# Kernel optimization log

Measured on AMD Instinct MI355X. Metric: run time of the kernel, lower is better.

## Reference

```python
import jax, jax.numpy as jnp
import numpy as np

EMB = 1024
HEADS = 16
HEAD_DIM = EMB // HEADS
ROPE_BASE = 10000.0


def rotate_half(x):
    # Interleaved rotate: pairs (x0,x1,x2,x3,...) -> (-x1,x0,-x3,x2,...)
    x1 = x[..., ::2]
    x2 = x[..., 1::2]
    return jnp.stack((-x2, x1), axis=-1).reshape(x.shape)


def rope_cos_sin(seq_len, head_dim):
    inv_freq = 1.0 / (ROPE_BASE ** (jnp.arange(0, head_dim, 2, dtype=jnp.float32) / head_dim))
    pos = jnp.arange(seq_len, dtype=jnp.float32)
    freqs = jnp.outer(pos, inv_freq)            # [S, hd/2]
    emb = jnp.concatenate([freqs, freqs], -1)   # [S, hd]  (NOTE: concat, matching source)
    return jnp.cos(emb)[None, None], jnp.sin(emb)[None, None]  # [1,1,S,hd]


def setup_inputs() -> dict:
    key = jax.random.key(0)
    ks = jax.random.split(key, 5)
    B, S = 2, 2048
    x = jax.random.normal(ks[0], (B, S, EMB), dtype=jnp.float32)
    scale = EMB ** -0.5
    Wq = jax.random.normal(ks[1], (EMB, EMB), dtype=jnp.float32) * scale
    Wk = jax.random.normal(ks[2], (EMB, EMB), dtype=jnp.float32) * scale
    Wv = jax.random.normal(ks[3], (EMB, EMB), dtype=jnp.float32) * scale
    Wo = jax.random.normal(ks[4], (EMB, EMB), dtype=jnp.float32) * scale
    return {"x": x, "Wq": Wq, "Wk": Wk, "Wv": Wv, "Wo": Wo}


def reference(x, Wq, Wk, Wv, Wo):
    B, S, E = x.shape
    def shape_heads(t):
        return t.reshape(B, S, HEADS, HEAD_DIM).transpose(0, 2, 1, 3)  # [B,H,S,hd]
    q = shape_heads(x @ Wq.T)
    k = shape_heads(x @ Wk.T)
    v = shape_heads(x @ Wv.T)
    cos, sin = rope_cos_sin(S, HEAD_DIM)
    q = q * cos + rotate_half(q) * sin
    k = k * cos + rotate_half(k) * sin
    scale = HEAD_DIM ** -0.5
    scores = jnp.einsum('bhqd,bhkd->bhqk', q, k) * scale  # [B,H,S,S]
    causal = jnp.triu(jnp.ones((S, S), dtype=bool), k=1)
    scores = jnp.where(causal, -jnp.inf, scores)
    attn = jax.nn.softmax(scores, axis=-1)
    out = jnp.einsum('bhqk,bhkd->bhqd', attn, v)           # [B,H,S,hd]
    out = out.transpose(0, 2, 1, 3).reshape(B, S, E)
    return out @ Wo.T
```

## Files before the change

kernel.cpp:

```cpp
#include <hip/hip_runtime.h>
#include <cstdint>
#include <cstddef>

typedef __bf16 bf16;
typedef __attribute__((ext_vector_type(8))) __bf16 bf16x8;
typedef __attribute__((ext_vector_type(4))) __bf16 bf16x4;
typedef __attribute__((ext_vector_type(4))) float f32x4;

constexpr int kS = 2048;
constexpr int kH = 16;
constexpr int kD = 64;

__device__ __forceinline__ void gload16(const bf16* g, bf16* l) {
  __builtin_amdgcn_global_load_lds((const __attribute__((address_space(1))) void*)g,
                                   (__attribute__((address_space(3))) void*)l, 16, 0, 0);
}

__global__ __launch_bounds__(256) void cast_all_kernel(
    const float* __restrict__ x, const float* __restrict__ wq, const float* __restrict__ wk,
    const float* __restrict__ wv, const float* __restrict__ wo,
    bf16* __restrict__ xb, bf16* __restrict__ wqb, bf16* __restrict__ wkb,
    bf16* __restrict__ wvb, bf16* __restrict__ wob) {
  int idx = blockIdx.x * 256 + threadIdx.x;
  const float* src; bf16* dst; int i;
  if (idx < (1 << 20)) { src = x; dst = xb; i = idx << 2; }
  else {
    int r = idx - (1 << 20);
    int t = r >> 18;
    i = (r & ((1 << 18) - 1)) << 2;
    src = (t == 0) ? wq : (t == 1) ? wk : (t == 2) ? wv : wo;
    dst = (t == 0) ? wqb : (t == 1) ? wkb : (t == 2) ? wvb : wob;
  }
  float4 v = *(const float4*)(src + i);
  bf16x4 o;
  o[0] = (bf16)v.x; o[1] = (bf16)v.y; o[2] = (bf16)v.z; o[3] = (bf16)v.w;
  *(bf16x4*)(dst + i) = o;
}


#define GSTAGE(BUF, KT)                                    \
  gload16(aP0 + (KT), &As[BUF][(w * 64 + l) * 8]);         \
  gload16(aP1 + (KT), &As[BUF][((4 + w) * 64 + l) * 8]);   \
  gload16(bP0 + (KT), &Bs[BUF][(w * 64 + l) * 8]);         \
  gload16(bP1 + (KT), &Bs[BUF][((4 + w) * 64 + l) * 8]);

__global__ __launch_bounds__(256) void gemm_qkv(const bf16* __restrict__ A,
                                                const bf16* __restrict__ wq,
                                                const bf16* __restrict__ wk,
                                                const bf16* __restrict__ wv,
                                                bf16* __restrict__ qo,
                                                bf16* __restrict__ ko,
                                                bf16* __restrict__ vto) {
  __shared__ bf16 As[2][128 * 32];
  __shared__ bf16 Bs[2][128 * 32];
  const int tid = threadIdx.x;
  const int w = tid >> 6, l = tid & 63;
  const int wr = w >> 1, wc = w & 1;
  const int lr = l & 15, lg = l >> 4;

  const int fid = (blockIdx.x & 7) * 96 + (blockIdx.x >> 3);
  const int mblk = fid & 31;
  const int ntile = fid >> 5;
  const int which = ntile >> 3;
  const int m0 = mblk * 128;
  const int n0 = (ntile & 7) * 128;
  const bf16* Bw = (which == 0) ? wq : (which == 1) ? wk : wv;

  const int srow = l >> 2;
  const int skcol = ((l & 3) ^ ((l >> 3) & 3)) << 3;
  const int K = 1024;

  const bf16* aP0 = A + (size_t)(m0 + w * 16 + srow) * K + skcol;
  const bf16* aP1 = A + (size_t)(m0 + 64 + w * 16 + srow) * K + skcol;
  const bf16* bP0 = Bw + (size_t)(n0 + w * 16 + srow) * K + skcol;
  const bf16* bP1 = Bw + (size_t)(n0 + 64 + w * 16 + srow) * K + skcol;

  f32x4 acc[4][4] = {};
  const int ca = (lg ^ ((lr >> 1) & 3)) * 8;

  GSTAGE(0, 0)
  __syncthreads();
  int cur = 0;
  for (int kt = 0; kt < K; kt += 32) {
    if (kt + 32 < K) { GSTAGE(cur ^ 1, kt + 32) }
    bf16x8 af[4], bfg[4];
#pragma unroll
    for (int mi = 0; mi < 4; mi++)
      af[mi] = *(const bf16x8*)&As[cur][(wr * 64 + mi * 16 + lr) * 32 + ca];
#pragma unroll
    for (int ni = 0; ni < 4; ni++)
      bfg[ni] = *(const bf16x8*)&Bs[cur][(wc * 64 + ni * 16 + lr) * 32 + ca];
    __builtin_amdgcn_s_setprio(1);
#pragma unroll
    for (int mi = 0; mi < 4; mi++)
#pragma unroll
      for (int ni = 0; ni < 4; ni++)
        acc[mi][ni] = __builtin_amdgcn_mfma_f32_16x16x32_bf16(af[mi], bfg[ni], acc[mi][ni], 0, 0, 0);
    __builtin_amdgcn_s_setprio(0);
    __syncthreads();
    cur ^= 1;
  }

  float invf_[4];
#pragma unroll
  for (int ni = 0; ni < 4; ni++) {
    int d31 = ((n0 + wc * 64 + ni * 16 + lr) & 63) & 31;
    invf_[ni] = exp2f((float)d31 * -0.41524100480466348f);
  }

#pragma unroll
  for (int mi = 0; mi < 4; mi++) {
#pragma unroll
    for (int ni = 0; ni < 4; ni++) {
#pragma unroll
      for (int r = 0; r < 4; r++) {
        const int m = m0 + wr * 64 + mi * 16 + lg * 4 + r;
        const int n = n0 + wc * 64 + ni * 16 + lr;
        float v = acc[mi][ni][r];
        const int st = m & 2047;
        const size_t bh = (size_t)(m >> 11) * kH + (n >> 6);
        if (which < 2) {
          float vp = __shfl_xor(v, 1);
          const int d = n & 63;
          float th = (float)st * invf_[ni];
          float sth = __sinf(th), cth = __cosf(th);
          float rv = v * cth + ((d & 1) ? vp : -vp) * sth;
          bf16* dst = which ? ko : qo;
          dst[((bh << 11) + st) * kD + (n & 63)] = (bf16)rv;
        } else {
          int pos = (st & ~31) | (((st >> 2) & 3) << 3) | (((st >> 4) & 1) << 2) | (st & 3);
          vto[((bh * kD + (n & 63)) << 11) + pos] = (bf16)v;
        }
      }
    }
  }
}

__global__ __launch_bounds__(256) void gemm_out(const bf16* __restrict__ A,
                                                const bf16* __restrict__ Bw,
                                                float* __restrict__ Cout) {
  __shared__ bf16 As[2][128 * 32];
  __shared__ bf16 Bs[2][128 * 32];
  const int tid = threadIdx.x;
  const int w = tid >> 6, l = tid & 63;
  const int wr = w >> 1, wc = w & 1;
  const int lr = l & 15, lg = l >> 4;
  const int m0 = blockIdx.y * 128, n0 = blockIdx.x * 128;
  const int K = 1024, N = 1024;

  const int srow = l >> 2;
  const int skcol = ((l & 3) ^ ((l >> 3) & 3)) << 3;

  const bf16* aP0 = A + (size_t)(m0 + w * 16 + srow) * K + skcol;
  const bf16* aP1 = A + (size_t)(m0 + 64 + w * 16 + srow) * K + skcol;
  const bf16* bP0 = Bw + (size_t)(n0 + w * 16 + srow) * K + skcol;
  const bf16* bP1 = Bw + (size_t)(n0 + 64 + w * 16 + srow) * K + skcol;

  f32x4 acc[4][4] = {};
  const int ca = (lg ^ ((lr >> 1) & 3)) * 8;

  GSTAGE(0, 0)
  __syncthreads();
  int cur = 0;
  for (int kt = 0; kt < K; kt += 32) {
    if (kt + 32 < K) { GSTAGE(cur ^ 1, kt + 32) }
    bf16x8 af[4], bfg[4];
#pragma unroll
    for (int mi = 0; mi < 4; mi++)
      af[mi] = *(const bf16x8*)&As[cur][(wr * 64 + mi * 16 + lr) * 32 + ca];
#pragma unroll
    for (int ni = 0; ni < 4; ni++)
      bfg[ni] = *(const bf16x8*)&Bs[cur][(wc * 64 + ni * 16 + lr) * 32 + ca];
    __builtin_amdgcn_s_setprio(1);
#pragma unroll
    for (int mi = 0; mi < 4; mi++)
#pragma unroll
      for (int ni = 0; ni < 4; ni++)
        acc[mi][ni] = __builtin_amdgcn_mfma_f32_16x16x32_bf16(af[mi], bfg[ni], acc[mi][ni], 0, 0, 0);
    __builtin_amdgcn_s_setprio(0);
    __syncthreads();
    cur ^= 1;
  }

#pragma unroll
  for (int mi = 0; mi < 4; mi++)
#pragma unroll
    for (int ni = 0; ni < 4; ni++)
#pragma unroll
      for (int r = 0; r < 4; r++) {
        const int m = m0 + wr * 64 + mi * 16 + lg * 4 + r;
        const int n = n0 + wc * 64 + ni * 16 + lr;
        Cout[(size_t)m * N + n] = acc[mi][ni][r];
      }
}


#define STAGE(BUF, KV0)                                                                  \
  {                                                                                      \
    const bf16* kg_ = kh + (size_t)((KV0) + w * 16 + lr) * 64 + lg * 8;                  \
    gload16(kg_,      &Ks[BUF][(w * 2 + 0) * 512 + l * 8]);                              \
    gload16(kg_ + 32, &Ks[BUF][(w * 2 + 1) * 512 + l * 8]);                              \
    const bf16* vg_ = vh + (size_t)(w * 16 + lr) * 2048 + (KV0) + lg * 8;                \
    gload16(vg_,      &Vs[BUF][(w * 2 + 0) * 512 + l * 8]);                              \
    gload16(vg_ + 32, &Vs[BUF][(w * 2 + 1) * 512 + l * 8]);                              \
  }

#define COMPUTE(BUF, DIAG, O, MRUN, LPART, QF, QROW, KVB)                                \
  {                                                                                      \
    bf16x8 kf_[4][2], vf_[4][2];                                                         \
    _Pragma("unroll") for (int s_ = 0; s_ < 4; s_++)                                     \
      _Pragma("unroll") for (int c_ = 0; c_ < 2; c_++)                                   \
        kf_[s_][c_] = *(const bf16x8*)&Ks[BUF][(s_ * 2 + c_) * 512 + l * 8];             \
    _Pragma("unroll") for (int c_ = 0; c_ < 4; c_++)                                     \
      _Pragma("unroll") for (int f_ = 0; f_ < 2; f_++)                                   \
        vf_[c_][f_] = *(const bf16x8*)&Vs[BUF][(c_ * 2 + f_) * 512 + l * 8];             \
    f32x4 sa_[4] = {};                                                                   \
    __builtin_amdgcn_s_setprio(1);                                                       \
    _Pragma("unroll") for (int s_ = 0; s_ < 4; s_++) {                                   \
      sa_[s_] = __builtin_amdgcn_mfma_f32_16x16x32_bf16(kf_[s_][0], QF[0], sa_[s_], 0, 0, 0); \
      sa_[s_] = __builtin_amdgcn_mfma_f32_16x16x32_bf16(kf_[s_][1], QF[1], sa_[s_], 0, 0, 0); \
    }                                                                                    \
    __builtin_amdgcn_s_setprio(0);                                                       \
    float sc_[4][4];                                                                     \
    float tml_ = -1e30f;                                                                 \
    _Pragma("unroll") for (int s_ = 0; s_ < 4; s_++)                                     \
      _Pragma("unroll") for (int r_ = 0; r_ < 4; r_++) {                                 \
        float v_ = sa_[s_][r_] * 0.125f;                                                 \
        if (DIAG) {                                                                      \
          int kk_ = (KVB) + s_ * 16 + lg * 4 + r_;                                       \
          v_ = (kk_ <= (QROW)) ? v_ : -1e30f;                                            \
        }                                                                                \
        sc_[s_][r_] = v_;                                                                \
        tml_ = fmaxf(tml_, v_);                                                          \
      }                                                                                  \
    if (__any(tml_ > MRUN + 20.0f)) {                                                    \
      float tm_ = tml_;                                                                  \
      tm_ = fmaxf(tm_, __shfl_xor(tm_, 16));                                             \
      tm_ = fmaxf(tm_, __shfl_xor(tm_, 32));                                             \
      tm_ = fmaxf(tm_, MRUN);                                                            \
      float f_ = __expf(MRUN - tm_);                                                     \
      _Pragma("unroll") for (int c_ = 0; c_ < 4; c_++) O[c_] *= f_;                      \
      LPART *= f_;                                                                       \
      MRUN = tm_;                                                                        \
    }                                                                                    \
    bf16x8 pf_[2];                                                                       \
    float ts_ = 0.0f;                                                                    \
    _Pragma("unroll") for (int s_ = 0; s_ < 4; s_++)                                     \
      _Pragma("unroll") for (int r_ = 0; r_ < 4; r_++) {                                 \
        float e_ = __expf(sc_[s_][r_] - MRUN);                                           \
        ts_ += e_;                                                                       \
        pf_[s_ >> 1][(s_ & 1) * 4 + r_] = (bf16)e_;                                      \
      }                                                                                  \
    LPART += ts_;                                                                        \
    __builtin_amdgcn_s_setprio(1);                                                       \
    _Pragma("unroll") for (int c_ = 0; c_ < 4; c_++) {                                   \
      O[c_] = __builtin_amdgcn_mfma_f32_16x16x32_bf16(vf_[c_][0], pf_[0], O[c_], 0, 0, 0); \
      O[c_] = __builtin_amdgcn_mfma_f32_16x16x32_bf16(vf_[c_][1], pf_[1], O[c_], 0, 0, 0); \
    }                                                                                    \
    __builtin_amdgcn_s_setprio(0);                                                       \
  }

#define EPILOG(O, LPART, Q0)                                                             \
  {                                                                                      \
    float lt_ = LPART;                                                                   \
    lt_ += __shfl_xor(lt_, 16);                                                          \
    lt_ += __shfl_xor(lt_, 32);                                                          \
    const float inv_ = 1.0f / lt_;                                                       \
    _Pragma("unroll") for (int c_ = 0; c_ < 4; c_++) {                                   \
      bf16x4 ov_;                                                                        \
      _Pragma("unroll") for (int r_ = 0; r_ < 4; r_++) ov_[r_] = (bf16)(O[c_][r_] * inv_); \
      size_t addr_ = ((size_t)(b * kS + (Q0) + lr)) * (kH * kD) + h * 64 + c_ * 16 + lg * 4; \
      *(bf16x4*)&ob[addr_] = ov_;                                                        \
    }                                                                                    \
  }

__global__ __launch_bounds__(256, 2) void attn_kernel(const bf16* __restrict__ qb,
                                                      const bf16* __restrict__ kb,
                                                      const bf16* __restrict__ vtb,
                                                      bf16* __restrict__ ob) {
  __shared__ bf16 Ks[2][4096];
  __shared__ bf16 Vs[2][4096];
  const int tid = threadIdx.x;
  const int w = tid >> 6, l = tid & 63;
  const int lr = l & 15, lg = l >> 4;
  const int bid = blockIdx.x;
  const int bh = bid & 31;
  const int p = bid >> 5;
  const int qtA = 31 - p, qtB = p;
  const bf16* qh = qb + (size_t)bh * (kS * kD);
  const bf16* kh = kb + (size_t)bh * (kS * kD);
  const bf16* vh = vtb + (size_t)bh * (kS * kD);
  const int b = bh >> 4, h = bh & 15;

  STAGE(0, 0)
  __syncthreads();
  int cur = 0;

  {
    const int q0 = qtA * 64 + w * 16;
    const int q = q0 + lr;
    bf16x8 qf[2];
#pragma unroll
    for (int c = 0; c < 2; c++)
      qf[c] = *(const bf16x8*)&qh[(size_t)(q0 + lr) * kD + c * 32 + lg * 8];
    float m_run = 8.0f, lpart = 0.0f;
    f32x4 o[4] = {};
    for (int t = 0; t <= qtA; t++) {
      STAGE(cur ^ 1, (t < qtA) ? (t + 1) * 64 : 0)
      COMPUTE(cur, (t == qtA), o, m_run, lpart, qf, q, t * 64)
      __syncthreads();
      cur ^= 1;
    }
    EPILOG(o, lpart, q0)
  }

  {
    const int q0 = qtB * 64 + w * 16;
    const int q = q0 + lr;
    bf16x8 qf[2];
#pragma unroll
    for (int c = 0; c < 2; c++)
      qf[c] = *(const bf16x8*)&qh[(size_t)(q0 + lr) * kD + c * 32 + lg * 8];
    float m_run = 8.0f, lpart = 0.0f;
    f32x4 o[4] = {};
    for (int t = 0; t <= qtB; t++) {
      if (t < qtB) STAGE(cur ^ 1, (t + 1) * 64)
      COMPUTE(cur, (t == qtB), o, m_run, lpart, qf, q, t * 64)
      __syncthreads();
      cur ^= 1;
    }
    EPILOG(o, lpart, q0)
  }
}

extern "C" void kernel_launch(void* const* d_in, const int* in_sizes, int n_in,
                              void* d_out, int out_size, void* d_ws, size_t ws_size,
                              hipStream_t stream) {
  const float* x  = (const float*)d_in[0];
  const float* wq = (const float*)d_in[1];
  const float* wk = (const float*)d_in[2];
  const float* wv = (const float*)d_in[3];
  const float* wo = (const float*)d_in[4];

  bf16* xb  = (bf16*)d_ws;
  bf16* qb  = xb + (1 << 22);
  bf16* kb  = qb + (1 << 22);
  bf16* vtb = kb + (1 << 22);
  bf16* ab  = vtb + (1 << 22);
  bf16* wqb = ab + (1 << 22);
  bf16* wkb = wqb + (1 << 20);
  bf16* wvb = wkb + (1 << 20);
  bf16* wob = wvb + (1 << 20);

  cast_all_kernel<<<8192, 256, 0, stream>>>(x, wq, wk, wv, wo, xb, wqb, wkb, wvb, wob);
  gemm_qkv<<<768, 256, 0, stream>>>(xb, wqb, wkb, wvb, qb, kb, vtb);
  attn_kernel<<<512, 256, 0, stream>>>(qb, kb, vtb, ab);
  gemm_out<<<dim3(8, 32), 256, 0, stream>>>(ab, wob, (float*)d_out);
}
```

Measured before the change: 127.9 us.

## Triple-buffer GEMM and attention K/V staging with vmcnt-based waits

```diff
diff --git a/kernel.cpp b/kernel.cpp
--- a/kernel.cpp
+++ b/kernel.cpp
@@ -44,6 +44,28 @@
   gload16(bP0 + (KT), &Bs[BUF][(w * 64 + l) * 8]);         \
   gload16(bP1 + (KT), &Bs[BUF][((4 + w) * 64 + l) * 8]);
 
+#define GEMM_KLOOP                                                                   \
+  GSTAGE(0, 0)                                                                       \
+  GSTAGE(1, 32)                                                                      \
+  for (int it = 0; it < 32; ++it) {                                                  \
+    if (it < 31) asm volatile("s_waitcnt vmcnt(4)" ::: "memory");                    \
+    else         asm volatile("s_waitcnt vmcnt(0)" ::: "memory");                    \
+    __builtin_amdgcn_s_barrier();                                                    \
+    if (it + 2 < 32) { GSTAGE((it + 2) % 3, (it + 2) * 32) }                         \
+    const bf16* Abuf = As[it % 3];                                                   \
+    const bf16* Bbuf = Bs[it % 3];                                                   \
+    bf16x8 af[4], bfg[4];                                                            \
+    _Pragma("unroll") for (int mi = 0; mi < 4; mi++)                                 \
+      af[mi] = *(const bf16x8*)&Abuf[(wr * 64 + mi * 16 + lr) * 32 + ca];            \
+    _Pragma("unroll") for (int ni = 0; ni < 4; ni++)                                 \
+      bfg[ni] = *(const bf16x8*)&Bbuf[(wc * 64 + ni * 16 + lr) * 32 + ca];           \
+    __builtin_amdgcn_s_setprio(1);                                                   \
+    _Pragma("unroll") for (int mi = 0; mi < 4; mi++)                                 \
+      _Pragma("unroll") for (int ni = 0; ni < 4; ni++)                               \
+        acc[mi][ni] = __builtin_amdgcn_mfma_f32_16x16x32_bf16(af[mi], bfg[ni], acc[mi][ni], 0, 0, 0); \
+    __builtin_amdgcn_s_setprio(0);                                                   \
+  }
+
 __global__ __launch_bounds__(256) void gemm_qkv(const bf16* __restrict__ A,
                                                 const bf16* __restrict__ wq,
                                                 const bf16* __restrict__ wk,
@@ -51,8 +73,8 @@
                                                 bf16* __restrict__ qo,
                                                 bf16* __restrict__ ko,
                                                 bf16* __restrict__ vto) {
-  __shared__ bf16 As[2][128 * 32];
-  __shared__ bf16 Bs[2][128 * 32];
+  __shared__ bf16 As[3][128 * 32];
+  __shared__ bf16 Bs[3][128 * 32];
   const int tid = threadIdx.x;
   const int w = tid >> 6, l = tid & 63;
   const int wr = w >> 1, wc = w & 1;
@@ -78,28 +100,7 @@
   f32x4 acc[4][4] = {};
   const int ca = (lg ^ ((lr >> 1) & 3)) * 8;
 
-  GSTAGE(0, 0)
-  __syncthreads();
-  int cur = 0;
-  for (int kt = 0; kt < K; kt += 32) {
-    if (kt + 32 < K) { GSTAGE(cur ^ 1, kt + 32) }
-    bf16x8 af[4], bfg[4];
-#pragma unroll
-    for (int mi = 0; mi < 4; mi++)
-      af[mi] = *(const bf16x8*)&As[cur][(wr * 64 + mi * 16 + lr) * 32 + ca];
-#pragma unroll
-    for (int ni = 0; ni < 4; ni++)
-      bfg[ni] = *(const bf16x8*)&Bs[cur][(wc * 64 + ni * 16 + lr) * 32 + ca];
-    __builtin_amdgcn_s_setprio(1);
-#pragma unroll
-    for (int mi = 0; mi < 4; mi++)
-#pragma unroll
-      for (int ni = 0; ni < 4; ni++)
-        acc[mi][ni] = __builtin_amdgcn_mfma_f32_16x16x32_bf16(af[mi], bfg[ni], acc[mi][ni], 0, 0, 0);
-    __builtin_amdgcn_s_setprio(0);
-    __syncthreads();
-    cur ^= 1;
-  }
+  GEMM_KLOOP
 
   float invf_[4];
 #pragma unroll
@@ -139,8 +140,8 @@
 __global__ __launch_bounds__(256) void gemm_out(const bf16* __restrict__ A,
                                                 const bf16* __restrict__ Bw,
                                                 float* __restrict__ Cout) {
-  __shared__ bf16 As[2][128 * 32];
-  __shared__ bf16 Bs[2][128 * 32];
+  __shared__ bf16 As[3][128 * 32];
+  __shared__ bf16 Bs[3][128 * 32];
   const int tid = threadIdx.x;
   const int w = tid >> 6, l = tid & 63;
   const int wr = w >> 1, wc = w & 1;
@@ -159,28 +160,7 @@
   f32x4 acc[4][4] = {};
   const int ca = (lg ^ ((lr >> 1) & 3)) * 8;
 
-  GSTAGE(0, 0)
-  __syncthreads();
-  int cur = 0;
-  for (int kt = 0; kt < K; kt += 32) {
-    if (kt + 32 < K) { GSTAGE(cur ^ 1, kt + 32) }
-    bf16x8 af[4], bfg[4];
-#pragma unroll
-    for (int mi = 0; mi < 4; mi++)
-      af[mi] = *(const bf16x8*)&As[cur][(wr * 64 + mi * 16 + lr) * 32 + ca];
-#pragma unroll
-    for (int ni = 0; ni < 4; ni++)
-      bfg[ni] = *(const bf16x8*)&Bs[cur][(wc * 64 + ni * 16 + lr) * 32 + ca];
-    __builtin_amdgcn_s_setprio(1);
-#pragma unroll
-    for (int mi = 0; mi < 4; mi++)
-#pragma unroll
-      for (int ni = 0; ni < 4; ni++)
-        acc[mi][ni] = __builtin_amdgcn_mfma_f32_16x16x32_bf16(af[mi], bfg[ni], acc[mi][ni], 0, 0, 0);
-    __builtin_amdgcn_s_setprio(0);
-    __syncthreads();
-    cur ^= 1;
-  }
+  GEMM_KLOOP
 
 #pragma unroll
   for (int mi = 0; mi < 4; mi++)
@@ -278,8 +258,8 @@
                                                       const bf16* __restrict__ kb,
                                                       const bf16* __restrict__ vtb,
                                                       bf16* __restrict__ ob) {
-  __shared__ bf16 Ks[2][4096];
-  __shared__ bf16 Vs[2][4096];
+  __shared__ bf16 Ks[3][4096];
+  __shared__ bf16 Vs[3][4096];
   const int tid = threadIdx.x;
   const int w = tid >> 6, l = tid & 63;
   const int lr = l & 15, lg = l >> 4;
@@ -287,50 +267,46 @@
   const int bh = bid & 31;
   const int p = bid >> 5;
   const int qtA = 31 - p, qtB = p;
+  const int nA = qtA + 1;
   const bf16* qh = qb + (size_t)bh * (kS * kD);
   const bf16* kh = kb + (size_t)bh * (kS * kD);
   const bf16* vh = vtb + (size_t)bh * (kS * kD);
   const int b = bh >> 4, h = bh & 15;
 
+  const int q0A = qtA * 64 + w * 16, q0B = qtB * 64 + w * 16;
+  const int qA = q0A + lr, qB = q0B + lr;
+  bf16x8 qfA[2], qfB[2];
+#pragma unroll
+  for (int c = 0; c < 2; c++) {
+    qfA[c] = *(const bf16x8*)&qh[(size_t)(q0A + lr) * kD + c * 32 + lg * 8];
+    qfB[c] = *(const bf16x8*)&qh[(size_t)(q0B + lr) * kD + c * 32 + lg * 8];
+  }
+
+  float mA = 8.0f, lA = 0.0f, mB = 8.0f, lB = 0.0f;
+  f32x4 oA[4] = {}, oB[4] = {};
+
   STAGE(0, 0)
-  __syncthreads();
-  int cur = 0;
-
-  {
-    const int q0 = qtA * 64 + w * 16;
-    const int q = q0 + lr;
-    bf16x8 qf[2];
-#pragma unroll
-    for (int c = 0; c < 2; c++)
-      qf[c] = *(const bf16x8*)&qh[(size_t)(q0 + lr) * kD + c * 32 + lg * 8];
-    float m_run = 8.0f, lpart = 0.0f;
-    f32x4 o[4] = {};
-    for (int t = 0; t <= qtA; t++) {
-      STAGE(cur ^ 1, (t < qtA) ? (t + 1) * 64 : 0)
-      COMPUTE(cur, (t == qtA), o, m_run, lpart, qf, q, t * 64)
-      __syncthreads();
-      cur ^= 1;
+  STAGE(1, 64)
+  for (int it = 0; it < 33; ++it) {
+    if (it < 32) asm volatile("s_waitcnt vmcnt(4)" ::: "memory");
+    else         asm volatile("s_waitcnt vmcnt(0)" ::: "memory");
+    __builtin_amdgcn_s_barrier();
+    if (it + 2 < 33) {
+      const int i2 = it + 2;
+      const int kv2 = (i2 < nA ? i2 : i2 - nA) * 64;
+      STAGE(i2 % 3, kv2)
     }
-    EPILOG(o, lpart, q0)
-  }
-
-  {
-    const int q0 = qtB * 64 + w * 16;
-    const int q = q0 + lr;
-    bf16x8 qf[2];
-#pragma unroll
-    for (int c = 0; c < 2; c++)
-      qf[c] = *(const bf16x8*)&qh[(size_t)(q0 + lr) * kD + c * 32 + lg * 8];
-    float m_run = 8.0f, lpart = 0.0f;
-    f32x4 o[4] = {};
-    for (int t = 0; t <= qtB; t++) {
-      if (t < qtB) STAGE(cur ^ 1, (t + 1) * 64)
-      COMPUTE(cur, (t == qtB), o, m_run, lpart, qf, q, t * 64)
-      __syncthreads();
-      cur ^= 1;
+    const int buf = it % 3;
+    if (it < nA) {
+      COMPUTE(buf, (it == qtA), oA, mA, lA, qfA, qA, it * 64)
+    } else {
+      const int tb = it - nA;
+      COMPUTE(buf, (it == 32), oB, mB, lB, qfB, qB, tb * 64)
     }
-    EPILOG(o, lpart, q0)
-  }
+  }
+
+  EPILOG(oA, lA, q0A)
+  EPILOG(oB, lB, q0B)
 }
 
 extern "C" void kernel_launch(void* const* d_in, const int* in_sizes, int n_in,
```

After: 139.1 us. 8.8% more time.
